# Optimization experiments

Hardware: AMD Instinct MI355X
Metric: run time of the kernel (lower is better)

## Reference

```python
import jax, jax.numpy as jnp
import numpy as np

B, T = 32, 512
LATENT, COND, HIDDEN, OUT, E = 64, 448, 1024, 512, 8
INPUT = LATENT + COND            # 512
INTER = LATENT + COND + HIDDEN   # 1536
GATE_H = 64


def setup_inputs() -> dict:
    key = jax.random.key(0)
    ks = jax.random.split(key, 20)
    d = {
        "z": jax.random.normal(ks[0], (B, T, LATENT), dtype=jnp.float32),
        "c": jax.random.normal(ks[1], (B, T, COND), dtype=jnp.float32),
    }
    # expert weights: kaiming-uniform-ish init, biases filled with 0.01 (as in torch code)
    layer_dims = [(INPUT, HIDDEN), (INTER, HIDDEN), (INTER, HIDDEN), (INTER, HIDDEN), (INTER, OUT)]
    for i, (fin, fout) in enumerate(layer_dims):
        bound = float(np.sqrt(6.0 / fin))
        d[f"w{i}"] = jax.random.uniform(ks[2 + i], (E, fin, fout), dtype=jnp.float32, minval=-bound, maxval=bound)
        d[f"b{i}"] = jnp.full((E, fout), 0.01, dtype=jnp.float32)
    # gate MLP: input_size -> 64 -> 64 -> E (stored as [in, out])
    gate_dims = [(INPUT, GATE_H), (GATE_H, GATE_H), (GATE_H, E)]
    for i, (fin, fout) in enumerate(gate_dims):
        bound = float(np.sqrt(1.0 / fin))
        d[f"gw{i}"] = jax.random.uniform(ks[10 + 2 * i], (fin, fout), dtype=jnp.float32, minval=-bound, maxval=bound)
        d[f"gb{i}"] = jax.random.uniform(ks[11 + 2 * i], (fout,), dtype=jnp.float32, minval=-bound, maxval=bound)
    return d


def reference(z, c, w0, b0, w1, b1, w2, b2, w3, b3, w4, b4, gw0, gb0, gw1, gb1, gw2, gb2):
    # gate -> per-token softmax mixing coefficients  [B, T, E]
    x = jnp.concatenate([z, c], axis=-1)
    h = jax.nn.leaky_relu(x @ gw0 + gb0)
    h = jax.nn.leaky_relu(h @ gw1 + gb1)
    coef = jax.nn.softmax(h @ gw2 + gb2, axis=-1)
    # Original computes mixed_weight for every t but baddbmm uses only mixed_weight[:, 0];
    # so the effective per-sequence weight uses coefficients at t=0 only (same math, no huge intermediate).
    coef0 = coef[:, 0]  # [B, E]
    layer_out = c
    layers = [(w0, b0, True), (w1, b1, True), (w2, b2, True), (w3, b3, True), (w4, b4, False)]
    for i, (w, b, act) in enumerate(layers):
        if i == 0:
            inp = jnp.concatenate([z, layer_out], axis=-1)      # [B, T, INPUT]
        else:
            inp = jnp.concatenate([z, c, layer_out], axis=-1)   # [B, T, INTER]
        wm = jnp.einsum('be,eio->bio', coef0, w)                # per-sequence mixed weight
        bm = jnp.einsum('bte,eo->bto', coef, b)                 # per-token mixed bias
        out = bm + jnp.einsum('bti,bio->bto', inp, wm)
        layer_out = jax.nn.leaky_relu(out) if act else out
    return layer_out
```

## Files before the change

### kernel.cpp

```cpp
#include <hip/hip_runtime.h>
#include <math.h>

#define B_     32
#define T_     512
#define LATENT 64
#define COND   448
#define HIDDEN 1024
#define OUTD   512
#define E_     8
#define INPUT_ 512
#define INTER_ 1536
#define GATEH  64
#define NTOK   (B_ * T_)
#define KTAIL  32

typedef __attribute__((ext_vector_type(8))) short short8;
typedef __attribute__((ext_vector_type(4))) float f32x4;

static __device__ __forceinline__ unsigned short f2bf(float x) {
    unsigned u = __float_as_uint(x);
    u += 0x7fffu + ((u >> 16) & 1u);
    return (unsigned short)(u >> 16);
}

__global__ __launch_bounds__(256) void wprep_kernel(
    const float* __restrict__ gw0, const float* __restrict__ gw1,
    unsigned short* __restrict__ gw0T, unsigned short* __restrict__ gw1T)
{
    int idx = blockIdx.x * 256 + threadIdx.x;
    if (idx < GATEH * INPUT_) {
        int n = idx >> 9, k = idx & 511;
        gw0T[n * INPUT_ + k] = f2bf(gw0[k * GATEH + n]);
    } else {
        int i2 = idx - GATEH * INPUT_;
        if (i2 < GATEH * GATEH) {
            int n = i2 >> 6, k = i2 & 63;
            gw1T[n * GATEH + k] = f2bf(gw1[k * GATEH + n]);
        }
    }
}

__global__ __launch_bounds__(256) void gate_kernel(
    const float* __restrict__ z, const float* __restrict__ c,
    const float* __restrict__ gb0,
    const float* __restrict__ gb1,
    const float* __restrict__ gw2, const float* __restrict__ gb2,
    const unsigned short* __restrict__ gw0T,
    const unsigned short* __restrict__ gw1T,
    float* __restrict__ coef, unsigned short* __restrict__ coefpad,
    unsigned short* __restrict__ xzb)
{
    __shared__ unsigned short Hb[GATEH][72];
    __shared__ float H2[GATEH][65];
    __shared__ float sLg[GATEH][E_];

    const int tid = threadIdx.x;
    const int lane = tid & 63;
    const int wv = tid >> 6;
    const int tok0 = blockIdx.x * 64;

#pragma unroll
    for (int i = 0; i < 4; ++i) {
        int idx = i * 256 + tid;
        int tr = idx >> 4, c4 = (idx & 15) * 4;
        float4 v = *(const float4*)(z + ((size_t)(tok0 + tr) * LATENT) + c4);
        ushort4 o = {f2bf(v.x), f2bf(v.y), f2bf(v.z), f2bf(v.w)};
        *(ushort4*)(xzb + (size_t)(tok0 + tr) * INPUT_ + c4) = o;
    }
#pragma unroll
    for (int i = 0; i < 28; ++i) {
        int idx = i * 256 + tid;
        int tr = idx / 112, c4 = (idx % 112) * 4;
        float4 v = *(const float4*)(c + ((size_t)(tok0 + tr) * COND) + c4);
        ushort4 o = {f2bf(v.x), f2bf(v.y), f2bf(v.z), f2bf(v.w)};
        *(ushort4*)(xzb + (size_t)(tok0 + tr) * INPUT_ + LATENT + c4) = o;
    }
    __threadfence_block();
    __syncthreads();

    const int fr = lane & 15, fq = lane >> 4;
    const int wm0 = (wv & 1) * 32, wn0 = (wv >> 1) * 32;

    f32x4 acc[2][2];
#pragma unroll
    for (int im = 0; im < 2; ++im)
#pragma unroll
        for (int in = 0; in < 2; ++in) acc[im][in] = (f32x4){0.f,0.f,0.f,0.f};

    for (int k0 = 0; k0 < INPUT_; k0 += 32) {
        short8 af[2], bf[2];
#pragma unroll
        for (int im = 0; im < 2; ++im)
            af[im] = *(const short8*)(xzb + (size_t)(tok0 + wm0 + im*16 + fr) * INPUT_
                                          + k0 + fq * 8);
#pragma unroll
        for (int in = 0; in < 2; ++in)
            bf[in] = *(const short8*)(gw0T + (size_t)(wn0 + in*16 + fr) * INPUT_
                                           + k0 + fq * 8);
#pragma unroll
        for (int im = 0; im < 2; ++im)
#pragma unroll
            for (int in = 0; in < 2; ++in)
                acc[im][in] = __builtin_amdgcn_mfma_f32_16x16x32_bf16(
                    af[im], bf[in], acc[im][in], 0, 0, 0);
    }
#pragma unroll
    for (int im = 0; im < 2; ++im)
#pragma unroll
        for (int in = 0; in < 2; ++in)
#pragma unroll
            for (int reg = 0; reg < 4; ++reg) {
                int m = wm0 + im*16 + fq*4 + reg;
                int n = wn0 + in*16 + fr;
                float h = acc[im][in][reg] + gb0[n];
                h = h > 0.f ? h : 0.01f * h;
                Hb[m][n] = f2bf(h);
            }
    __syncthreads();

    f32x4 a2[2][2];
#pragma unroll
    for (int im = 0; im < 2; ++im)
#pragma unroll
        for (int in = 0; in < 2; ++in) a2[im][in] = (f32x4){0.f,0.f,0.f,0.f};
#pragma unroll
    for (int k0 = 0; k0 < GATEH; k0 += 32) {
        short8 af[2], bf[2];
#pragma unroll
        for (int im = 0; im < 2; ++im)
            af[im] = *(const short8*)(&Hb[wm0 + im*16 + fr][k0 + fq*8]);
#pragma unroll
        for (int in = 0; in < 2; ++in)
            bf[in] = *(const short8*)(gw1T + (size_t)(wn0 + in*16 + fr) * GATEH
                                           + k0 + fq * 8);
#pragma unroll
        for (int im = 0; im < 2; ++im)
#pragma unroll
            for (int in = 0; in < 2; ++in)
                a2[im][in] = __builtin_amdgcn_mfma_f32_16x16x32_bf16(
                    af[im], bf[in], a2[im][in], 0, 0, 0);
    }
#pragma unroll
    for (int im = 0; im < 2; ++im)
#pragma unroll
        for (int in = 0; in < 2; ++in)
#pragma unroll
            for (int reg = 0; reg < 4; ++reg) {
                int m = wm0 + im*16 + fq*4 + reg;
                int n = wn0 + in*16 + fr;
                float h = a2[im][in][reg] + gb1[n];
                H2[m][n] = h > 0.f ? h : 0.01f * h;
            }
    __syncthreads();

    {
        int tok = tid >> 2, e0 = (tid & 3) * 2;
        float l0 = gb2[e0], l1 = gb2[e0 + 1];
#pragma unroll
        for (int i = 0; i < GATEH; ++i) {
            float h = H2[tok][i];
            l0 = fmaf(h, gw2[i * E_ + e0], l0);
            l1 = fmaf(h, gw2[i * E_ + e0 + 1], l1);
        }
        sLg[tok][e0] = l0; sLg[tok][e0 + 1] = l1;
    }
    __syncthreads();

    if (tid < 64) {
        int token = tok0 + tid;
        float lg[E_], m = -1e30f, s = 0.f;
#pragma unroll
        for (int e = 0; e < E_; ++e) { lg[e] = sLg[tid][e]; m = fmaxf(m, lg[e]); }
#pragma unroll
        for (int e = 0; e < E_; ++e) { lg[e] = expf(lg[e] - m); s += lg[e]; }
        float inv = 1.f / s;
        unsigned short pad[KTAIL];
#pragma unroll
        for (int e = 0; e < E_; ++e) {
            float cv = lg[e] * inv;
            coef[(size_t)token * E_ + e] = cv;
            pad[e] = f2bf(cv);
        }
#pragma unroll
        for (int j = E_; j < KTAIL; ++j) pad[j] = 0;
#pragma unroll
        for (int q = 0; q < 4; ++q)
            *(ushort4*)(coefpad + (size_t)token * KTAIL + q * 4) =
                *(const ushort4*)&pad[q * 4];
    }
}

#define MI 32
#define MO 64
#define MP 65

__global__ __launch_bounds__(256) void mixT_kernel(
    const float* __restrict__ w,
    const float* __restrict__ bias,
    const float* __restrict__ coef,
    unsigned short* __restrict__ wmT,
    int fin, int fout, int gb, int batch0)
{
    __shared__ float sW[E_][MI][MP];
    __shared__ float sC[B_][E_];
    const int t = threadIdx.x;
    const int fin_tot = fin + KTAIL;
    const int nbi = fin / MI;
    const int i0 = (blockIdx.x % nbi) * MI;
    const int o0 = (blockIdx.x / nbi) * MO;

    if (t < gb * E_)
        sC[t >> 3][t & 7] = coef[(size_t)(batch0 + (t >> 3)) * T_ * E_ + (t & 7)];

#pragma unroll
    for (int r = 0; r < 64; ++r) {
        int idx = r * 256 + t;
        int o = idx & 63;
        int i = (idx >> 6) & 31;
        int e = idx >> 11;
        sW[e][i][o] = w[(size_t)e * fin * fout + (size_t)(i0 + i) * fout + o0 + o];
    }
    __syncthreads();

    const int o  = t >> 2;
    const int i8 = (t & 3) * 8;
    for (int b = 0; b < gb; ++b) {
        float v[8];
#pragma unroll
        for (int j = 0; j < 8; ++j) v[j] = 0.f;
#pragma unroll
        for (int e = 0; e < E_; ++e) {
            float cc = sC[b][e];
#pragma unroll
            for (int j = 0; j < 8; ++j)
                v[j] = fmaf(cc, sW[e][i8 + j][o], v[j]);
        }
        unsigned short u[8];
#pragma unroll
        for (int j = 0; j < 8; ++j) u[j] = f2bf(v[j]);
        *(int4*)(wmT + ((size_t)b * fout + o0 + o) * fin_tot + i0 + i8) = *(const int4*)u;
    }

    if (i0 == 0) {
        const int jj = t & 3;
        unsigned short u[8];
#pragma unroll
        for (int q = 0; q < 8; ++q)
            u[q] = (jj == 0) ? f2bf(bias[(size_t)q * fout + o0 + o]) : 0;
        for (int b = 0; b < gb; ++b)
            *(int4*)(wmT + ((size_t)b * fout + o0 + o) * fin_tot + fin + jj * 8) =
                *(const int4*)u;
    }
}

__global__ __launch_bounds__(256, 3) void gemm_kernel(
    const unsigned short* __restrict__ xz,
    const unsigned short* __restrict__ prev,
    const unsigned short* __restrict__ wmT,
    const unsigned short* __restrict__ coefpad,
    float* __restrict__ outf,
    unsigned short* __restrict__ outb,
    int fin_tot, int fout, int act, int batch0)
{
    __shared__ __align__(16) unsigned short As[128 * 32];
    __shared__ __align__(16) unsigned short Bs[128 * 32];

    const int tid = threadIdx.x;
    const int lane = tid & 63;
    const int wv = tid >> 6;
    const int row0 = blockIdx.y * 128;
    const int col0 = blockIdx.x * 128;
    const size_t tokbase = (size_t)(batch0 + blockIdx.z) * T_;
    const unsigned short* wmb = wmT + (size_t)blockIdx.z * fin_tot * fout;

    f32x4 acc[4][4];
#pragma unroll
    for (int im = 0; im < 4; ++im)
#pragma unroll
        for (int in = 0; in < 4; ++in)
            acc[im][in] = (f32x4){0.f, 0.f, 0.f, 0.f};

    const int lrow = lane >> 2;
    const int lk8  = (((lane & 3) ^ ((lane >> 3) & 3)) * 8);
    const int wm0 = (wv & 1) * 64, wn0 = (wv >> 1) * 64;
    const int fr = lane & 15, fq = lane >> 4;
    const int koff = (fq ^ ((fr >> 1) & 3)) * 8;
    const int ktail0 = fin_tot - KTAIL;

    for (int k0 = 0; k0 < fin_tot; k0 += 32) {
        const unsigned short* abase; int astr, acol;
        if (k0 < INPUT_)       { abase = xz;      astr = INPUT_; acol = k0; }
        else if (k0 < ktail0)  { abase = prev;    astr = HIDDEN; acol = k0 - INPUT_; }
        else                   { abase = coefpad; astr = KTAIL;  acol = 0; }

        __syncthreads();
#pragma unroll
        for (int q = 0; q < 4; ++q) {
            int ch = wv * 4 + q;
            const unsigned short* src;
            unsigned short* dst;
            if (ch < 8) {
                int m = ch * 16 + lrow;
                src = abase + (tokbase + row0 + m) * astr + acol + lk8;
                dst = As + ch * 512;
            } else {
                int n = (ch - 8) * 16 + lrow;
                src = wmb + (size_t)(col0 + n) * fin_tot + k0 + lk8;
                dst = Bs + (ch - 8) * 512;
            }
            __builtin_amdgcn_global_load_lds(
                (const __attribute__((address_space(1))) unsigned int*)(const void*)src,
                (__attribute__((address_space(3))) unsigned int*)(void*)dst,
                16, 0, 0);
        }
        __syncthreads();

        short8 af[4], bfv[4];
#pragma unroll
        for (int im = 0; im < 4; ++im)
            af[im] = *(const short8*)(As + (wm0 / 16 + im) * 512 + fr * 32 + koff);
#pragma unroll
        for (int in = 0; in < 4; ++in)
            bfv[in] = *(const short8*)(Bs + (wn0 / 16 + in) * 512 + fr * 32 + koff);
#pragma unroll
        for (int im = 0; im < 4; ++im)
#pragma unroll
            for (int in = 0; in < 4; ++in)
                acc[im][in] = __builtin_amdgcn_mfma_f32_16x16x32_bf16(
                    af[im], bfv[in], acc[im][in], 0, 0, 0);
    }

#pragma unroll
    for (int im = 0; im < 4; ++im) {
#pragma unroll
        for (int in = 0; in < 4; ++in) {
#pragma unroll
            for (int reg = 0; reg < 4; ++reg) {
                int r = wm0 + im * 16 + fq * 4 + reg;
                int col = wn0 + in * 16 + fr;
                float v = acc[im][in][reg];
                if (act) v = v > 0.f ? v : 0.01f * v;
                size_t off = (tokbase + row0 + r) * fout + col0 + col;
                if (outb) outb[off] = f2bf(v);
                else      outf[off] = v;
            }
        }
    }
}

extern "C" void kernel_launch(void* const* d_in, const int* in_sizes, int n_in,
                              void* d_out, int out_size, void* d_ws, size_t ws_size,
                              hipStream_t stream)
{
    const float* z = (const float*)d_in[0];
    const float* c = (const float*)d_in[1];
    const float* w[5]  = {(const float*)d_in[2], (const float*)d_in[4],
                          (const float*)d_in[6], (const float*)d_in[8],
                          (const float*)d_in[10]};
    const float* bs[5] = {(const float*)d_in[3], (const float*)d_in[5],
                          (const float*)d_in[7], (const float*)d_in[9],
                          (const float*)d_in[11]};
    const float* gw0 = (const float*)d_in[12]; const float* gb0 = (const float*)d_in[13];
    const float* gw1 = (const float*)d_in[14]; const float* gb1 = (const float*)d_in[15];
    const float* gw2 = (const float*)d_in[16]; const float* gb2 = (const float*)d_in[17];

    const size_t g0t_b  = (size_t)GATEH * INPUT_ * 2;
    const size_t g1t_b  = (size_t)GATEH * GATEH * 2;
    const size_t xz_b   = (size_t)NTOK * INPUT_ * 2;
    const size_t coef_b = (size_t)NTOK * E_ * 4;
    const size_t cpad_b = (size_t)NTOK * KTAIL * 2;
    const size_t act_b  = (size_t)NTOK * HIDDEN * 2;
    const size_t wmun   = (size_t)(INTER_ + KTAIL) * HIDDEN * 2;

    char* p = (char*)d_ws;
    unsigned short* gw0T  = (unsigned short*)p;  p += g0t_b;
    unsigned short* gw1T  = (unsigned short*)p;  p += g1t_b;
    unsigned short* xzb   = (unsigned short*)p;  p += xz_b;
    float*          coef  = (float*)p;           p += coef_b;
    unsigned short* cpad  = (unsigned short*)p;  p += cpad_b;
    unsigned short* actB  = (unsigned short*)p;  p += act_b;

    size_t base = g0t_b + g1t_b + xz_b + coef_b + cpad_b + act_b;
    size_t avail = (ws_size > base) ? ws_size - base : 0;

    int gb;
    unsigned short* actA;
    unsigned short* wmT;
    if (avail >= act_b + 32 * wmun) {
        gb = 32; actA = (unsigned short*)p; p += act_b; wmT = (unsigned short*)p;
    } else {
        actA = (unsigned short*)d_out;
        wmT  = (unsigned short*)p;
        gb = 1;
        for (int g = 16; g >= 2; g >>= 1)
            if (avail >= (size_t)g * wmun) { gb = g; break; }
    }

    wprep_kernel<<<(GATEH * (INPUT_ + GATEH) + 255) / 256, 256, 0, stream>>>(
        gw0, gw1, gw0T, gw1T);
    gate_kernel<<<NTOK / 64, 256, 0, stream>>>(
        z, c, gb0, gb1, gw2, gb2, gw0T, gw1T, coef, cpad, xzb);

    struct L { int fin, fout, act; const unsigned short* in; unsigned short* outb; };
    L Ls[5] = {
        {INPUT_, HIDDEN, 1, actB , actA},
        {INTER_, HIDDEN, 1, actA, actB},
        {INTER_, HIDDEN, 1, actB, actA},
        {INTER_, HIDDEN, 1, actA, actB},
        {INTER_, OUTD,   0, actB, 0},
    };

    for (int Li = 0; Li < 5; ++Li) {
        int fin = Ls[Li].fin, fout = Ls[Li].fout;
        int nblk = (fin / MI) * (fout / MO);
        for (int g = 0; g < B_; g += gb) {
            mixT_kernel<<<nblk, 256, 0, stream>>>(
                w[Li], bs[Li], coef, wmT, fin, fout, gb, g);
            gemm_kernel<<<dim3(fout / 128, T_ / 128, gb), 256, 0, stream>>>(
                xzb, Ls[Li].in, wmT, cpad,
                (float*)d_out, Ls[Li].outb, fin + KTAIL, fout, Ls[Li].act, g);
        }
    }
}
```

Before: 717.2 us.

## Pre-transpose expert weights to bf16, simplify mixing, deepen GEMM K-tile to 64

Adds a kernel that converts each layer's expert weights once into transposed bf16 layout. The mixing kernel then becomes a simple per-thread vectorized combine with no shared-memory transpose and half the weight read bytes. The GEMM now stages a 64-deep K slice per iteration, halving barriers per MAC, and KTAIL grows to 64 to stay aligned. It also uses a 1D swizzled block mapping for L2 locality and raises occupancy hints to 4 blocks per CU. The cost is more workspace, doubled LDS per block, and extra transpose launches.

Result: slower. 791.0 us (+10.3%).

```diff
diff --git a/kernel.cpp b/kernel.cpp
--- a/kernel.cpp
+++ b/kernel.cpp
@@ -12,7 +12,7 @@
 #define INTER_ 1536
 #define GATEH  64
 #define NTOK   (B_ * T_)
-#define KTAIL  32
+#define KTAIL  64
 
 typedef __attribute__((ext_vector_type(8))) short short8;
 typedef __attribute__((ext_vector_type(4))) float f32x4;
@@ -21,6 +21,9 @@
     unsigned u = __float_as_uint(x);
     u += 0x7fffu + ((u >> 16) & 1u);
     return (unsigned short)(u >> 16);
+}
+static __device__ __forceinline__ float bf2f(unsigned short b) {
+    return __uint_as_float((unsigned)b << 16);
 }
 
 __global__ __launch_bounds__(256) void wprep_kernel(
@@ -40,6 +43,40 @@
     }
 }
 
+__global__ __launch_bounds__(256) void wtrans_kernel(
+    const float* __restrict__ w, unsigned short* __restrict__ wT,
+    int fin, int fout)
+{
+    __shared__ unsigned short sT[32][266];
+    const int t = threadIdx.x;
+    const int nit = fin >> 8;
+    const int nio = nit * (fout >> 5);
+    const int e = blockIdx.x / nio;
+    const int rem = blockIdx.x % nio;
+    const int i0 = (rem % nit) * 256;
+    const int o0 = (rem / nit) * 32;
+    const float* we = w + (size_t)e * fin * fout;
+
+#pragma unroll
+    for (int rr = 0; rr < 32; ++rr) {
+        int idx = rr * 256 + t;
+        int i = idx >> 5, o = idx & 31;
+        sT[o][i] = f2bf(we[(size_t)(i0 + i) * fout + o0 + o]);
+    }
+    __syncthreads();
+
+#pragma unroll
+    for (int pp = 0; pp < 4; ++pp) {
+        int o = pp * 8 + (t >> 5);
+        int i16 = (t & 31) * 8;
+        unsigned short u[8];
+#pragma unroll
+        for (int j = 0; j < 8; ++j) u[j] = sT[o][i16 + j];
+        *(int4*)(wT + ((size_t)e * fout + o0 + o) * fin + i0 + i16) =
+            *(const int4*)u;
+    }
+}
+
 __global__ __launch_bounds__(256) void gate_kernel(
     const float* __restrict__ z, const float* __restrict__ c,
     const float* __restrict__ gb0,
@@ -184,94 +221,104 @@
 #pragma unroll
         for (int j = E_; j < KTAIL; ++j) pad[j] = 0;
 #pragma unroll
-        for (int q = 0; q < 4; ++q)
+        for (int q = 0; q < KTAIL / 4; ++q)
             *(ushort4*)(coefpad + (size_t)token * KTAIL + q * 4) =
                 *(const ushort4*)&pad[q * 4];
     }
 }
 
-#define MI 32
-#define MO 64
-#define MP 65
-
-__global__ __launch_bounds__(256) void mixT_kernel(
-    const float* __restrict__ w,
+__global__ __launch_bounds__(256) void mix_kernel(
+    const unsigned short* __restrict__ wT,
     const float* __restrict__ bias,
     const float* __restrict__ coef,
     unsigned short* __restrict__ wmT,
     int fin, int fout, int gb, int batch0)
 {
-    __shared__ float sW[E_][MI][MP];
     __shared__ float sC[B_][E_];
     const int t = threadIdx.x;
     const int fin_tot = fin + KTAIL;
-    const int nbi = fin / MI;
-    const int i0 = (blockIdx.x % nbi) * MI;
-    const int o0 = (blockIdx.x / nbi) * MO;
-
     if (t < gb * E_)
         sC[t >> 3][t & 7] = coef[(size_t)(batch0 + (t >> 3)) * T_ * E_ + (t & 7)];
-
-#pragma unroll
-    for (int r = 0; r < 64; ++r) {
-        int idx = r * 256 + t;
-        int o = idx & 63;
-        int i = (idx >> 6) & 31;
-        int e = idx >> 11;
-        sW[e][i][o] = w[(size_t)e * fin * fout + (size_t)(i0 + i) * fout + o0 + o];
-    }
-    __syncthreads();
-
-    const int o  = t >> 2;
-    const int i8 = (t & 3) * 8;
-    for (int b = 0; b < gb; ++b) {
-        float v[8];
-#pragma unroll
-        for (int j = 0; j < 8; ++j) v[j] = 0.f;
+    __syncthreads();
+
+    int idx = blockIdx.x * 256 + t;
+    const int main_n = fout * (fin >> 3);
+    if (idx < main_n) {
+        const int o = idx / (fin >> 3);
+        const int i8 = (idx % (fin >> 3)) * 8;
+        float we[E_][8];
 #pragma unroll
         for (int e = 0; e < E_; ++e) {
-            float cc = sC[b][e];
+            int4 r = *(const int4*)(wT + ((size_t)e * fout + o) * fin + i8);
+            const unsigned* p = (const unsigned*)&r;
+#pragma unroll
+            for (int q = 0; q < 4; ++q) {
+                we[e][2*q]   = __uint_as_float(p[q] << 16);
+                we[e][2*q+1] = __uint_as_float(p[q] & 0xffff0000u);
+            }
+        }
+        for (int b = 0; b < gb; ++b) {
+            float v[8];
+#pragma unroll
+            for (int j = 0; j < 8; ++j) v[j] = 0.f;
+#pragma unroll
+            for (int e = 0; e < E_; ++e) {
+                float cc = sC[b][e];
+#pragma unroll
+                for (int j = 0; j < 8; ++j) v[j] = fmaf(cc, we[e][j], v[j]);
+            }
+            unsigned short u[8];
+#pragma unroll
+            for (int j = 0; j < 8; ++j) u[j] = f2bf(v[j]);
+            *(int4*)(wmT + ((size_t)b * fout + o) * fin_tot + i8) = *(const int4*)u;
+        }
+    } else {
+        int tix = idx - main_n;
+        if (tix < fout * (KTAIL >> 3)) {
+            const int o = tix >> 3;
+            const int q = tix & 7;
+            unsigned short u[8];
 #pragma unroll
             for (int j = 0; j < 8; ++j)
-                v[j] = fmaf(cc, sW[e][i8 + j][o], v[j]);
-        }
-        unsigned short u[8];
-#pragma unroll
-        for (int j = 0; j < 8; ++j) u[j] = f2bf(v[j]);
-        *(int4*)(wmT + ((size_t)b * fout + o0 + o) * fin_tot + i0 + i8) = *(const int4*)u;
-    }
-
-    if (i0 == 0) {
-        const int jj = t & 3;
-        unsigned short u[8];
-#pragma unroll
-        for (int q = 0; q < 8; ++q)
-            u[q] = (jj == 0) ? f2bf(bias[(size_t)q * fout + o0 + o]) : 0;
-        for (int b = 0; b < gb; ++b)
-            *(int4*)(wmT + ((size_t)b * fout + o0 + o) * fin_tot + fin + jj * 8) =
-                *(const int4*)u;
-    }
-}
-
-__global__ __launch_bounds__(256, 3) void gemm_kernel(
+                u[j] = (q == 0) ? f2bf(bias[(size_t)j * fout + o]) : 0;
+            for (int b = 0; b < gb; ++b)
+                *(int4*)(wmT + ((size_t)b * fout + o) * fin_tot + fin + q * 8) =
+                    *(const int4*)u;
+        }
+    }
+}
+
+__global__ __launch_bounds__(256, 4) void gemm_kernel(
     const unsigned short* __restrict__ xz,
     const unsigned short* __restrict__ prev,
     const unsigned short* __restrict__ wmT,
     const unsigned short* __restrict__ coefpad,
     float* __restrict__ outf,
     unsigned short* __restrict__ outb,
-    int fin_tot, int fout, int act, int batch0)
-{
-    __shared__ __align__(16) unsigned short As[128 * 32];
-    __shared__ __align__(16) unsigned short Bs[128 * 32];
+    int fin, int fout, int act, int batch0, int nx)
+{
+    __shared__ __align__(16) unsigned short As[128 * 64];
+    __shared__ __align__(16) unsigned short Bs[128 * 64];
 
     const int tid = threadIdx.x;
     const int lane = tid & 63;
     const int wv = tid >> 6;
-    const int row0 = blockIdx.y * 128;
-    const int col0 = blockIdx.x * 128;
-    const size_t tokbase = (size_t)(batch0 + blockIdx.z) * T_;
-    const unsigned short* wmb = wmT + (size_t)blockIdx.z * fin_tot * fout;
+
+    {
+    }
+    const int f = blockIdx.x;
+    const int r8 = f & 7;
+    const int q8 = f >> 3;
+    const int y = q8 & 3;
+    const int g = (q8 >> 2) * 8 + r8;
+    const int x = g % nx;
+    const int zb = g / nx;
+
+    const int fin_tot = fin + KTAIL;
+    const int row0 = y * 128;
+    const int col0 = x * 128;
+    const size_t tokbase = (size_t)(batch0 + zb) * T_;
+    const unsigned short* wmb = wmT + (size_t)zb * fin_tot * fout;
 
     f32x4 acc[4][4];
 #pragma unroll
@@ -285,49 +332,58 @@
     const int wm0 = (wv & 1) * 64, wn0 = (wv >> 1) * 64;
     const int fr = lane & 15, fq = lane >> 4;
     const int koff = (fq ^ ((fr >> 1) & 3)) * 8;
-    const int ktail0 = fin_tot - KTAIL;
-
-    for (int k0 = 0; k0 < fin_tot; k0 += 32) {
-        const unsigned short* abase; int astr, acol;
-        if (k0 < INPUT_)       { abase = xz;      astr = INPUT_; acol = k0; }
-        else if (k0 < ktail0)  { abase = prev;    astr = HIDDEN; acol = k0 - INPUT_; }
-        else                   { abase = coefpad; astr = KTAIL;  acol = 0; }
-
+
+    for (int k0 = 0; k0 < fin_tot; k0 += 64) {
         __syncthreads();
 #pragma unroll
         for (int q = 0; q < 4; ++q) {
-            int ch = wv * 4 + q;
-            const unsigned short* src;
-            unsigned short* dst;
-            if (ch < 8) {
-                int m = ch * 16 + lrow;
-                src = abase + (tokbase + row0 + m) * astr + acol + lk8;
-                dst = As + ch * 512;
-            } else {
-                int n = (ch - 8) * 16 + lrow;
-                src = wmb + (size_t)(col0 + n) * fin_tot + k0 + lk8;
-                dst = Bs + (ch - 8) * 512;
-            }
+            int ai = wv * 4 + q;
+            int ch = ai >> 1, h = ai & 1;
+            int kk = k0 + h * 32;
+            const unsigned short* abase; int astr, acol;
+            if (kk < INPUT_)      { abase = xz;      astr = INPUT_; acol = kk; }
+            else if (kk < fin)    { abase = prev;    astr = HIDDEN; acol = kk - INPUT_; }
+            else                  { abase = coefpad; astr = KTAIL;  acol = kk - fin; }
+            const unsigned short* src =
+                abase + (tokbase + row0 + ch * 16 + lrow) * astr + acol + lk8;
             __builtin_amdgcn_global_load_lds(
                 (const __attribute__((address_space(1))) unsigned int*)(const void*)src,
-                (__attribute__((address_space(3))) unsigned int*)(void*)dst,
+                (__attribute__((address_space(3))) unsigned int*)(void*)
+                    (As + ch * 1024 + h * 512),
                 16, 0, 0);
         }
+#pragma unroll
+        for (int q = 0; q < 4; ++q) {
+            int bi = wv * 4 + q;
+            int ch = bi >> 1, h = bi & 1;
+            const unsigned short* src =
+                wmb + (size_t)(col0 + ch * 16 + lrow) * fin_tot + k0 + h * 32 + lk8;
+            __builtin_amdgcn_global_load_lds(
+                (const __attribute__((address_space(1))) unsigned int*)(const void*)src,
+                (__attribute__((address_space(3))) unsigned int*)(void*)
+                    (Bs + ch * 1024 + h * 512),
+                16, 0, 0);
+        }
         __syncthreads();
 
-        short8 af[4], bfv[4];
-#pragma unroll
-        for (int im = 0; im < 4; ++im)
-            af[im] = *(const short8*)(As + (wm0 / 16 + im) * 512 + fr * 32 + koff);
-#pragma unroll
-        for (int in = 0; in < 4; ++in)
-            bfv[in] = *(const short8*)(Bs + (wn0 / 16 + in) * 512 + fr * 32 + koff);
-#pragma unroll
-        for (int im = 0; im < 4; ++im)
+#pragma unroll
+        for (int h = 0; h < 2; ++h) {
+            short8 af[4], bfv[4];
+#pragma unroll
+            for (int im = 0; im < 4; ++im)
+                af[im] = *(const short8*)(As + ((wm0 >> 4) + im) * 1024
+                                             + h * 512 + fr * 32 + koff);
 #pragma unroll
             for (int in = 0; in < 4; ++in)
-                acc[im][in] = __builtin_amdgcn_mfma_f32_16x16x32_bf16(
-                    af[im], bfv[in], acc[im][in], 0, 0, 0);
+                bfv[in] = *(const short8*)(Bs + ((wn0 >> 4) + in) * 1024
+                                              + h * 512 + fr * 32 + koff);
+#pragma unroll
+            for (int im = 0; im < 4; ++im)
+#pragma unroll
+                for (int in = 0; in < 4; ++in)
+                    acc[im][in] = __builtin_amdgcn_mfma_f32_16x16x32_bf16(
+                        af[im], bfv[in], acc[im][in], 0, 0, 0);
+        }
     }
 
 #pragma unroll
@@ -336,11 +392,11 @@
         for (int in = 0; in < 4; ++in) {
 #pragma unroll
             for (int reg = 0; reg < 4; ++reg) {
-                int r = wm0 + im * 16 + fq * 4 + reg;
+                int rr = wm0 + im * 16 + fq * 4 + reg;
                 int col = wn0 + in * 16 + fr;
                 float v = acc[im][in][reg];
                 if (act) v = v > 0.f ? v : 0.01f * v;
-                size_t off = (tokbase + row0 + r) * fout + col0 + col;
+                size_t off = (tokbase + row0 + rr) * fout + col0 + col;
                 if (outb) outb[off] = f2bf(v);
                 else      outf[off] = v;
             }
@@ -364,6 +420,9 @@
     const float* gw1 = (const float*)d_in[14]; const float* gb1 = (const float*)d_in[15];
     const float* gw2 = (const float*)d_in[16]; const float* gb2 = (const float*)d_in[17];
 
+    const int fins[5]  = {INPUT_, INTER_, INTER_, INTER_, INTER_};
+    const int fouts[5] = {HIDDEN, HIDDEN, HIDDEN, HIDDEN, OUTD};
+
     const size_t g0t_b  = (size_t)GATEH * INPUT_ * 2;
     const size_t g1t_b  = (size_t)GATEH * GATEH * 2;
     const size_t xz_b   = (size_t)NTOK * INPUT_ * 2;
@@ -375,12 +434,17 @@
     char* p = (char*)d_ws;
     unsigned short* gw0T  = (unsigned short*)p;  p += g0t_b;
     unsigned short* gw1T  = (unsigned short*)p;  p += g1t_b;
+    unsigned short* wT[5];
+    for (int L = 0; L < 5; ++L) {
+        wT[L] = (unsigned short*)p;
+        p += (size_t)E_ * fins[L] * fouts[L] * 2;
+    }
     unsigned short* xzb   = (unsigned short*)p;  p += xz_b;
     float*          coef  = (float*)p;           p += coef_b;
     unsigned short* cpad  = (unsigned short*)p;  p += cpad_b;
     unsigned short* actB  = (unsigned short*)p;  p += act_b;
 
-    size_t base = g0t_b + g1t_b + xz_b + coef_b + cpad_b + act_b;
+    size_t base = (size_t)(p - (char*)d_ws);
     size_t avail = (ws_size > base) ? ws_size - base : 0;
 
     int gb;
@@ -398,6 +462,10 @@
 
     wprep_kernel<<<(GATEH * (INPUT_ + GATEH) + 255) / 256, 256, 0, stream>>>(
         gw0, gw1, gw0T, gw1T);
+    for (int L = 0; L < 5; ++L) {
+        int nblk = E_ * (fins[L] >> 8) * (fouts[L] >> 5);
+        wtrans_kernel<<<nblk, 256, 0, stream>>>(w[L], wT[L], fins[L], fouts[L]);
+    }
     gate_kernel<<<NTOK / 64, 256, 0, stream>>>(
         z, c, gb0, gb1, gw2, gb2, gw0T, gw1T, coef, cpad, xzb);
 
@@ -412,13 +480,14 @@
 
     for (int Li = 0; Li < 5; ++Li) {
         int fin = Ls[Li].fin, fout = Ls[Li].fout;
-        int nblk = (fin / MI) * (fout / MO);
+        int mix_threads = fout * (fin >> 3) + fout * (KTAIL >> 3);
         for (int g = 0; g < B_; g += gb) {
-            mixT_kernel<<<nblk, 256, 0, stream>>>(
-                w[Li], bs[Li], coef, wmT, fin, fout, gb, g);
-            gemm_kernel<<<dim3(fout / 128, T_ / 128, gb), 256, 0, stream>>>(
+            mix_kernel<<<(mix_threads + 255) / 256, 256, 0, stream>>>(
+                wT[Li], bs[Li], coef, wmT, fin, fout, gb, g);
+            int nx = fout / 128;
+            gemm_kernel<<<nx * 4 * gb, 256, 0, stream>>>(
                 xzb, Ls[Li].in, wmT, cpad,
-                (float*)d_out, Ls[Li].outb, fin + KTAIL, fout, Ls[Li].act, g);
-        }
-    }
-}
+                (float*)d_out, Ls[Li].outb, fin, fout, Ls[Li].act, g, nx);
+        }
+    }
+}
```
